# Optimization experiments

Hardware: AMD Instinct MI355X
Metric: run time of the kernel (lower is better)

## Reference

```python
import jax, jax.numpy as jnp
import numpy as np

WINDOW = 128  # causal window width
D_SCALE = None  # set from val dim at trace time


def _softsign(x):
    return x / (1.0 + jnp.abs(x))


def setup_inputs() -> dict:
    key = jax.random.key(0)
    k1, k2 = jax.random.split(key)
    B, N, D = 4, 4096, 256
    val = jax.random.normal(k1, (B, N, D), dtype=jnp.float32)
    state = jax.random.normal(k2, (B, N), dtype=jnp.float32)
    return {"val": val, "state": state}


def reference(val, state):
    # val: [B, N, D], state: [B, N]
    B, N, D = val.shape
    # pairwise_fn: scaled dot product -> scores [B, N, N]
    scores = jnp.einsum('bnd,bmd->bnm', val, val) / jnp.sqrt(jnp.asarray(D, val.dtype))
    # edge_compress_fn: softsign
    edges = _softsign(scores)
    # causal window mask: source j satisfies (j <= i) & (j >= i - window)
    i = jnp.arange(N)[:, None]
    j = jnp.arange(N)[None, :]
    mask = (j <= i) & (j >= i - WINDOW)  # [N, N]
    edges = edges * mask[None, :, :].astype(edges.dtype)
    # val_proj_fn / state_proj_fn are Identity
    delta_state = jnp.einsum('bij,bj->bi', edges, state)   # [B, N]
    delta_val = jnp.einsum('bij,bjd->bid', edges, val)      # [B, N, D]
    return (delta_state, delta_val)
```

## Files before the change

kernel.cpp:

```cpp
#include <hip/hip_runtime.h>

#define NSEQ 4096
#define DIM  256
#define WIN  128
#define BATCH 4

typedef __bf16 bf16x8 __attribute__((ext_vector_type(8)));
typedef float  f32x4  __attribute__((ext_vector_type(4)));
typedef int    v2i    __attribute__((ext_vector_type(2)));
typedef int    v4i    __attribute__((ext_vector_type(4)));

__device__ __forceinline__ int sub_off(int j, int d) {
    return (((j >> 2) * 16 + (d >> 4)) << 6) + ((j & 3) << 4) + (d & 15);
}

__device__ __forceinline__ unsigned short f2bf(float f) {
    unsigned u = __builtin_bit_cast(unsigned, f);
    u += 0x7fffu + ((u >> 16) & 1u);
    return (unsigned short)(u >> 16);
}

__global__ __launch_bounds__(256, 2)
void sp_kernel(const float* __restrict__ val,
               const float* __restrict__ state,
               float* __restrict__ out) {
    __shared__ __align__(128) unsigned short buf[2][8192];
    __shared__ __align__(128) unsigned short E_s[32 * 56];
    __shared__ float ds_part[4][16];

    const int bx  = blockIdx.x;
    const int lbx = ((bx & 7) << 6) + (bx >> 3);
    const int b      = lbx >> 7;
    const int tile_i = lbx & 127;
    const int r0     = tile_i << 5;

    const int t   = threadIdx.x;
    const int w   = t >> 6;
    const int l   = t & 63;
    const int l15 = l & 15;
    const int l4  = l >> 4;
    const int mt  = w >> 1;
    const int jt  = w & 1;

    const float* valb = val + ((size_t)b * NSEQ) * DIM;
    const float* stb  = state + ((size_t)b * NSEQ);
    float* out_state  = out + ((size_t)b * NSEQ);
    float* out_val    = out + (size_t)BATCH * NSEQ + ((size_t)b * NSEQ) * DIM;

    const int s_jl[2] = {(w << 2) + l4, (w << 2) + l4 + 16};

    {
        const float* src = valb + ((size_t)tile_i << 13);
        #pragma unroll
        for (int p = 0; p < 8; ++p) {
            const int jl = s_jl[p & 1];
            const int d0 = (l15 << 2) + ((p >> 1) << 6);
            float4 v = *reinterpret_cast<const float4*>(src + jl * DIM + d0);
            ushort4 hh;
            hh.x = f2bf(v.x); hh.y = f2bf(v.y); hh.z = f2bf(v.z); hh.w = f2bf(v.w);
            *reinterpret_cast<ushort4*>(&buf[0][sub_off(jl, d0)]) = hh;
        }
    }
    __syncthreads();

    const int il = (mt << 4) + l15;
    const int jl = (jt << 4) + l15;
    bf16x8 af[8];
    #pragma unroll
    for (int ks = 0; ks < 8; ++ks)
        af[ks] = *reinterpret_cast<const bf16x8*>(&buf[0][sub_off(il, (l4 << 3) + (ks << 5))]);

    const int tj0 = (tile_i >= 4) ? (tile_i - 4) : 0;

    float dsacc[4] = {0.f, 0.f, 0.f, 0.f};
    f32x4 accpv[2][4];
    #pragma unroll
    for (int m2 = 0; m2 < 2; ++m2)
        #pragma unroll
        for (int tt = 0; tt < 4; ++tt)
            accpv[m2][tt] = (f32x4){0.f, 0.f, 0.f, 0.f};

    int p = 0;
    for (int ti = tile_i; ti >= tj0; --ti) {
        const unsigned short* bp = &buf[p][0];
        const bool havenext = (ti > tj0);

        float4 stg[8];
        if (havenext) {
            const float* src = valb + ((size_t)(ti - 1) << 13);
            #pragma unroll
            for (int q = 0; q < 8; ++q)
                stg[q] = *reinterpret_cast<const float4*>(src + s_jl[q & 1] * DIM
                                                          + (l15 << 2) + ((q >> 1) << 6));
        }

        bf16x8 sb[8];
        #pragma unroll
        for (int ks = 0; ks < 8; ++ks)
            sb[ks] = *reinterpret_cast<const bf16x8*>(&bp[sub_off(jl, (l4 << 3) + (ks << 5))]);
        f32x4 acc = (f32x4){0.f, 0.f, 0.f, 0.f};
        __builtin_amdgcn_s_setprio(1);
        #pragma unroll
        for (int ks = 0; ks < 8; ++ks)
            acc = __builtin_amdgcn_mfma_f32_16x16x32_bf16(af[ks], sb[ks], acc, 0, 0, 0);
        __builtin_amdgcn_s_setprio(0);

        const int jb = ti << 5;
        const int jg = jb + jl;
        const float stv = stb[jg];
        const int ib = r0 + (mt << 4) + (l4 << 2);
        #pragma unroll
        for (int r = 0; r < 4; ++r) {
            float s = acc[r] * 0.0625f;
            float e = s / (1.0f + fabsf(s));
            const int ig = ib + r;
            if (jg > ig || jg < ig - WIN) e = 0.0f;
            dsacc[r] += e * stv;
            E_s[((mt << 4) + (l4 << 2) + r) * 56 + (jt << 4) + l15] = f2bf(e);
        }

        if (havenext) {
            unsigned short* bn = &buf[1 - p][0];
            #pragma unroll
            for (int q = 0; q < 8; ++q) {
                ushort4 hh;
                hh.x = f2bf(stg[q].x); hh.y = f2bf(stg[q].y);
                hh.z = f2bf(stg[q].z); hh.w = f2bf(stg[q].w);
                *reinterpret_cast<ushort4*>(&bn[sub_off(s_jl[q & 1],
                                                        (l15 << 2) + ((q >> 1) << 6))]) = hh;
            }
        }
        __syncthreads();

        bf16x8 ef0 = *reinterpret_cast<const bf16x8*>(&E_s[l15 * 56 + (l4 << 3)]);
        bf16x8 ef1 = *reinterpret_cast<const bf16x8*>(&E_s[(16 + l15) * 56 + (l4 << 3)]);
        const unsigned lds_base = (unsigned)(size_t)bp;
        #pragma unroll
        for (int tt = 0; tt < 4; ++tt) {
            const int nt = (w << 2) + tt;
            unsigned a0 = lds_base + (unsigned)((((l4 << 5) + nt) << 7) + (l15 << 3));
            v2i t0, t1;
            asm volatile("ds_read_b64_tr_b16 %0, %1" : "=v"(t0) : "v"(a0) : "memory");
            asm volatile("ds_read_b64_tr_b16 %0, %1 offset:2048" : "=v"(t1) : "v"(a0) : "memory");
            asm volatile("s_waitcnt lgkmcnt(0)" ::: "memory");
            __builtin_amdgcn_sched_barrier(0);
            v4i tmp; tmp.x = t0.x; tmp.y = t0.y; tmp.z = t1.x; tmp.w = t1.y;
            bf16x8 bfr = __builtin_bit_cast(bf16x8, tmp);
            __builtin_amdgcn_s_setprio(1);
            accpv[0][tt] = __builtin_amdgcn_mfma_f32_16x16x32_bf16(ef0, bfr, accpv[0][tt], 0, 0, 0);
            accpv[1][tt] = __builtin_amdgcn_mfma_f32_16x16x32_bf16(ef1, bfr, accpv[1][tt], 0, 0, 0);
            __builtin_amdgcn_s_setprio(0);
        }
        if (havenext) __syncthreads();
        p ^= 1;
    }

    #pragma unroll
    for (int m = 1; m <= 8; m <<= 1) {
        #pragma unroll
        for (int r = 0; r < 4; ++r)
            dsacc[r] += __shfl_xor(dsacc[r], m, 64);
    }
    if (l15 == 0) {
        #pragma unroll
        for (int r = 0; r < 4; ++r)
            ds_part[w][(l4 << 2) + r] = dsacc[r];
    }
    __syncthreads();
    if (t < 32) {
        const int m2 = t >> 4;
        out_state[r0 + t] = ds_part[(m2 << 1)][t & 15] + ds_part[(m2 << 1) + 1][t & 15];
    }

    #pragma unroll
    for (int m2 = 0; m2 < 2; ++m2) {
        #pragma unroll
        for (int tt = 0; tt < 4; ++tt) {
            const int d = (w << 6) + (tt << 4) + l15;
            #pragma unroll
            for (int r = 0; r < 4; ++r) {
                const int ig = r0 + (m2 << 4) + (l4 << 2) + r;
                out_val[(size_t)ig * DIM + d] = accpv[m2][tt][r];
            }
        }
    }
}

extern "C" void kernel_launch(void* const* d_in, const int* in_sizes, int n_in,
                              void* d_out, int out_size, void* d_ws, size_t ws_size,
                              hipStream_t stream) {
    const float* val   = (const float*)d_in[0];
    const float* state = (const float*)d_in[1];
    float* out = (float*)d_out;
    sp_kernel<<<dim3(BATCH * (NSEQ / 32)), dim3(256), 0, stream>>>(val, state, out);
}
```

Before: 17.42 us.

## Triple-buffer val tiles and double-buffer edges to drop second barrier per iteration

Moves from two to three LDS val buffers and double-buffers the edge tile, which removes the trailing __syncthreads in each loop iteration. The B fragments for the next score MFMA are prefetched from the next buffer right after the barrier. All transposed LDS reads for the PV MFMAs are now issued before a single waitcnt, so they overlap. The cost is more LDS per block (about 52KB), which could reduce occupancy below 2 blocks per CU, and extra registers for the prefetched fragments.

```diff
diff --git a/kernel.cpp b/kernel.cpp
--- a/kernel.cpp
+++ b/kernel.cpp
@@ -24,8 +24,8 @@
 void sp_kernel(const float* __restrict__ val,
                const float* __restrict__ state,
                float* __restrict__ out) {
-    __shared__ __align__(128) unsigned short buf[2][8192];
-    __shared__ __align__(128) unsigned short E_s[32 * 56];
+    __shared__ __align__(128) unsigned short vbuf[3][8192];
+    __shared__ __align__(128) unsigned short E_s[2][32 * 56];
     __shared__ float ds_part[4][16];
 
     const int bx  = blockIdx.x;
@@ -58,19 +58,22 @@
             float4 v = *reinterpret_cast<const float4*>(src + jl * DIM + d0);
             ushort4 hh;
             hh.x = f2bf(v.x); hh.y = f2bf(v.y); hh.z = f2bf(v.z); hh.w = f2bf(v.w);
-            *reinterpret_cast<ushort4*>(&buf[0][sub_off(jl, d0)]) = hh;
+            *reinterpret_cast<ushort4*>(&vbuf[0][sub_off(jl, d0)]) = hh;
         }
     }
     __syncthreads();
 
     const int il = (mt << 4) + l15;
     const int jl = (jt << 4) + l15;
-    bf16x8 af[8];
-    #pragma unroll
-    for (int ks = 0; ks < 8; ++ks)
-        af[ks] = *reinterpret_cast<const bf16x8*>(&buf[0][sub_off(il, (l4 << 3) + (ks << 5))]);
-
-    const int tj0 = (tile_i >= 4) ? (tile_i - 4) : 0;
+    bf16x8 af[8], sb[8];
+    #pragma unroll
+    for (int ks = 0; ks < 8; ++ks) {
+        af[ks] = *reinterpret_cast<const bf16x8*>(&vbuf[0][sub_off(il, (l4 << 3) + (ks << 5))]);
+        sb[ks] = *reinterpret_cast<const bf16x8*>(&vbuf[0][sub_off(jl, (l4 << 3) + (ks << 5))]);
+    }
+
+    const int tj0   = (tile_i >= 4) ? (tile_i - 4) : 0;
+    const int ntile = tile_i - tj0 + 1;
 
     float dsacc[4] = {0.f, 0.f, 0.f, 0.f};
     f32x4 accpv[2][4];
@@ -80,24 +83,26 @@
         for (int tt = 0; tt < 4; ++tt)
             accpv[m2][tt] = (f32x4){0.f, 0.f, 0.f, 0.f};
 
-    int p = 0;
-    for (int ti = tile_i; ti >= tj0; --ti) {
-        const unsigned short* bp = &buf[p][0];
-        const bool havenext = (ti > tj0);
-
+    int bpi = 0;
+    for (int q = 0; q < ntile; ++q) {
+        const int ti = tile_i - q;
+        const bool havenext = (q + 1 < ntile);
+        const int bni = (bpi == 2) ? 0 : bpi + 1;
+        const unsigned short* bp = &vbuf[bpi][0];
+        unsigned short* bn = &vbuf[bni][0];
+        unsigned short* Ecur = &E_s[q & 1][0];
+
+        const int jg = (ti << 5) + jl;
+        const float stv = stb[jg];
         float4 stg[8];
         if (havenext) {
             const float* src = valb + ((size_t)(ti - 1) << 13);
             #pragma unroll
-            for (int q = 0; q < 8; ++q)
-                stg[q] = *reinterpret_cast<const float4*>(src + s_jl[q & 1] * DIM
-                                                          + (l15 << 2) + ((q >> 1) << 6));
-        }
-
-        bf16x8 sb[8];
-        #pragma unroll
-        for (int ks = 0; ks < 8; ++ks)
-            sb[ks] = *reinterpret_cast<const bf16x8*>(&bp[sub_off(jl, (l4 << 3) + (ks << 5))]);
+            for (int qq = 0; qq < 8; ++qq)
+                stg[qq] = *reinterpret_cast<const float4*>(src + s_jl[qq & 1] * DIM
+                                                           + (l15 << 2) + ((qq >> 1) << 6));
+        }
+
         f32x4 acc = (f32x4){0.f, 0.f, 0.f, 0.f};
         __builtin_amdgcn_s_setprio(1);
         #pragma unroll
@@ -105,9 +110,6 @@
             acc = __builtin_amdgcn_mfma_f32_16x16x32_bf16(af[ks], sb[ks], acc, 0, 0, 0);
         __builtin_amdgcn_s_setprio(0);
 
-        const int jb = ti << 5;
-        const int jg = jb + jl;
-        const float stv = stb[jg];
         const int ib = r0 + (mt << 4) + (l4 << 2);
         #pragma unroll
         for (int r = 0; r < 4; ++r) {
@@ -116,43 +118,51 @@
             const int ig = ib + r;
             if (jg > ig || jg < ig - WIN) e = 0.0f;
             dsacc[r] += e * stv;
-            E_s[((mt << 4) + (l4 << 2) + r) * 56 + (jt << 4) + l15] = f2bf(e);
+            Ecur[((mt << 4) + (l4 << 2) + r) * 56 + (jt << 4) + l15] = f2bf(e);
         }
 
         if (havenext) {
-            unsigned short* bn = &buf[1 - p][0];
-            #pragma unroll
-            for (int q = 0; q < 8; ++q) {
+            #pragma unroll
+            for (int qq = 0; qq < 8; ++qq) {
                 ushort4 hh;
-                hh.x = f2bf(stg[q].x); hh.y = f2bf(stg[q].y);
-                hh.z = f2bf(stg[q].z); hh.w = f2bf(stg[q].w);
-                *reinterpret_cast<ushort4*>(&bn[sub_off(s_jl[q & 1],
-                                                        (l15 << 2) + ((q >> 1) << 6))]) = hh;
+                hh.x = f2bf(stg[qq].x); hh.y = f2bf(stg[qq].y);
+                hh.z = f2bf(stg[qq].z); hh.w = f2bf(stg[qq].w);
+                *reinterpret_cast<ushort4*>(&bn[sub_off(s_jl[qq & 1],
+                                                        (l15 << 2) + ((qq >> 1) << 6))]) = hh;
             }
         }
         __syncthreads();
 
-        bf16x8 ef0 = *reinterpret_cast<const bf16x8*>(&E_s[l15 * 56 + (l4 << 3)]);
-        bf16x8 ef1 = *reinterpret_cast<const bf16x8*>(&E_s[(16 + l15) * 56 + (l4 << 3)]);
+        bf16x8 ef0 = *reinterpret_cast<const bf16x8*>(&Ecur[l15 * 56 + (l4 << 3)]);
+        bf16x8 ef1 = *reinterpret_cast<const bf16x8*>(&Ecur[(16 + l15) * 56 + (l4 << 3)]);
+        if (havenext) {
+            #pragma unroll
+            for (int ks = 0; ks < 8; ++ks)
+                sb[ks] = *reinterpret_cast<const bf16x8*>(&bn[sub_off(jl, (l4 << 3) + (ks << 5))]);
+        }
         const unsigned lds_base = (unsigned)(size_t)bp;
+        v2i tr[8];
         #pragma unroll
         for (int tt = 0; tt < 4; ++tt) {
             const int nt = (w << 2) + tt;
             unsigned a0 = lds_base + (unsigned)((((l4 << 5) + nt) << 7) + (l15 << 3));
-            v2i t0, t1;
-            asm volatile("ds_read_b64_tr_b16 %0, %1" : "=v"(t0) : "v"(a0) : "memory");
-            asm volatile("ds_read_b64_tr_b16 %0, %1 offset:2048" : "=v"(t1) : "v"(a0) : "memory");
-            asm volatile("s_waitcnt lgkmcnt(0)" ::: "memory");
-            __builtin_amdgcn_sched_barrier(0);
-            v4i tmp; tmp.x = t0.x; tmp.y = t0.y; tmp.z = t1.x; tmp.w = t1.y;
+            asm volatile("ds_read_b64_tr_b16 %0, %1" : "=v"(tr[2 * tt]) : "v"(a0) : "memory");
+            asm volatile("ds_read_b64_tr_b16 %0, %1 offset:2048" : "=v"(tr[2 * tt + 1]) : "v"(a0) : "memory");
+        }
+        asm volatile("s_waitcnt lgkmcnt(0)" ::: "memory");
+        __builtin_amdgcn_sched_barrier(0);
+        __builtin_amdgcn_s_setprio(1);
+        #pragma unroll
+        for (int tt = 0; tt < 4; ++tt) {
+            v4i tmp;
+            tmp.x = tr[2 * tt].x; tmp.y = tr[2 * tt].y;
+            tmp.z = tr[2 * tt + 1].x; tmp.w = tr[2 * tt + 1].y;
             bf16x8 bfr = __builtin_bit_cast(bf16x8, tmp);
-            __builtin_amdgcn_s_setprio(1);
             accpv[0][tt] = __builtin_amdgcn_mfma_f32_16x16x32_bf16(ef0, bfr, accpv[0][tt], 0, 0, 0);
             accpv[1][tt] = __builtin_amdgcn_mfma_f32_16x16x32_bf16(ef1, bfr, accpv[1][tt], 0, 0, 0);
-            __builtin_amdgcn_s_setprio(0);
-        }
-        if (havenext) __syncthreads();
-        p ^= 1;
+        }
+        __builtin_amdgcn_s_setprio(0);
+        bpi = bni;
     }
 
     #pragma unroll
```

Result: no change. 17.20 us (-1.3%).
